# Kernel tuning notes

Hardware: AMD Instinct MI355X
Metric: run time of the kernel (lower is better)

The kernel has to match this reference:

```python
import jax, jax.numpy as jnp
import numpy as np

IN_FEATURES = 4096
OUT_FEATURES = 14336
GROUP_SIZE = 128
EPS = 1e-6


def setup_inputs() -> dict:
    key = jax.random.key(0)
    k1, k2, k3, k4 = jax.random.split(key, 4)
    num_groups = IN_FEATURES // GROUP_SIZE
    x = jax.random.normal(k1, (8, IN_FEATURES), dtype=jnp.float32)
    weights_uint8 = jax.random.randint(k2, (OUT_FEATURES, IN_FEATURES), 0, 256, dtype=jnp.int32)
    # per-(out_row, group) [scale, min_val]; scale small so dequant weights are O(1)
    scales_min_vals = jax.random.normal(k3, (OUT_FEATURES * num_groups, 2), dtype=jnp.float32) * 0.01
    norm_weights = jnp.ones((IN_FEATURES,), dtype=jnp.float32)
    bias = jax.random.normal(k4, (OUT_FEATURES,), dtype=jnp.float32)
    return {
        "x": x,
        "weights_uint8": weights_uint8,
        "scales_min_vals": scales_min_vals,
        "norm_weights": norm_weights,
        "bias": bias,
    }


def _dequantize(weights_uint8, scales_min_vals):
    out_f, in_f = weights_uint8.shape
    ng = in_f // GROUP_SIZE
    smv = scales_min_vals.reshape(out_f, ng, 2)  # [O, G, 2]
    wq = weights_uint8.reshape(out_f, ng, GROUP_SIZE).astype(jnp.float32)
    # RTN dequant: w = q * scale + min_val, per group
    w = wq * smv[..., 0:1] + smv[..., 1:2]
    return w.reshape(out_f, in_f)


def _rmsnorm(x, norm_weights):
    var = jnp.mean(x * x, axis=-1, keepdims=True)
    return x * jax.lax.rsqrt(var + EPS) * norm_weights


def reference(x, weights_uint8, scales_min_vals, norm_weights, bias):
    xn = _rmsnorm(x, norm_weights)               # [B, I]
    w = _dequantize(weights_uint8, scales_min_vals)  # [O, I]
    return jnp.einsum('bi,oi->bo', xn, w) + bias  # [B, O]
```

## Files before the change

kernel.cpp:

```cpp
#include <hip/hip_runtime.h>

#define IN_F 4096
#define OUT_F 14336
#define NG 32
#define NB 8

__global__ __launch_bounds__(256) void rmsnorm_k(const float* __restrict__ x,
                                                 const float* __restrict__ nw,
                                                 float* __restrict__ xn) {
  const int b = blockIdx.x;
  const int t = threadIdx.x;
  const float* xr = x + b * IN_F;
  float4 v[4];
  float ss = 0.f;
#pragma unroll
  for (int i = 0; i < 4; ++i) {
    v[i] = reinterpret_cast<const float4*>(xr)[i * 256 + t];
    ss += v[i].x * v[i].x + v[i].y * v[i].y + v[i].z * v[i].z + v[i].w * v[i].w;
  }
#pragma unroll
  for (int m = 1; m < 64; m <<= 1) ss += __shfl_xor(ss, m, 64);
  __shared__ float red[4];
  if ((t & 63) == 0) red[t >> 6] = ss;
  __syncthreads();
  ss = red[0] + red[1] + red[2] + red[3];
  const float r = rsqrtf(ss * (1.0f / IN_F) + 1e-6f);
#pragma unroll
  for (int i = 0; i < 4; ++i) {
    float4 w = reinterpret_cast<const float4*>(nw)[i * 256 + t];
    float4 o;
    o.x = v[i].x * r * w.x;
    o.y = v[i].y * r * w.y;
    o.z = v[i].z * r * w.z;
    o.w = v[i].w * r * w.w;
    reinterpret_cast<float4*>(xn + b * IN_F)[i * 256 + t] = o;
  }
}

__global__ __launch_bounds__(256) void gemv_k(const int* __restrict__ W,
                                              const float2* __restrict__ smv,
                                              const float* __restrict__ xn,
                                              const float* __restrict__ bias,
                                              float* __restrict__ out) {
  const int t = threadIdx.x;
  const int lane = t & 63;
  const int wave = t >> 6;
  const int row0 = (blockIdx.x * 4 + wave) * 4;

  float acc[4][NB];
#pragma unroll
  for (int rr = 0; rr < 4; ++rr)
#pragma unroll
    for (int b = 0; b < NB; ++b) acc[rr][b] = 0.f;

  const int lcol = lane * 4;
  for (int k = 0; k < 16; ++k) {
    const int col = k * 256 + lcol;
    float4 xv[NB];
#pragma unroll
    for (int b = 0; b < NB; ++b)
      xv[b] = *reinterpret_cast<const float4*>(xn + b * IN_F + col);
    const int g = col >> 7;
#pragma unroll
    for (int rr = 0; rr < 4; ++rr) {
      const int o = row0 + rr;
      const int4 q = *reinterpret_cast<const int4*>(W + o * IN_F + col);
      const float2 sm = smv[o * NG + g];
      const float w0 = (float)q.x * sm.x + sm.y;
      const float w1 = (float)q.y * sm.x + sm.y;
      const float w2 = (float)q.z * sm.x + sm.y;
      const float w3 = (float)q.w * sm.x + sm.y;
#pragma unroll
      for (int b = 0; b < NB; ++b) {
        acc[rr][b] = fmaf(w0, xv[b].x, acc[rr][b]);
        acc[rr][b] = fmaf(w1, xv[b].y, acc[rr][b]);
        acc[rr][b] = fmaf(w2, xv[b].z, acc[rr][b]);
        acc[rr][b] = fmaf(w3, xv[b].w, acc[rr][b]);
      }
    }
  }

#pragma unroll
  for (int rr = 0; rr < 4; ++rr)
#pragma unroll
    for (int b = 0; b < NB; ++b) {
      float v = acc[rr][b];
#pragma unroll
      for (int m = 1; m < 64; m <<= 1) v += __shfl_xor(v, m, 64);
      acc[rr][b] = v;
    }

  if (lane < 32) {
    const int rr = lane >> 3;
    const int b = lane & 7;
    const int o = row0 + rr;
    out[b * OUT_F + o] = acc[rr][b] + bias[o];
  }
}

extern "C" void kernel_launch(void* const* d_in, const int* in_sizes, int n_in,
                              void* d_out, int out_size, void* d_ws, size_t ws_size,
                              hipStream_t stream) {
  const float* x = (const float*)d_in[0];
  const int* W = (const int*)d_in[1];
  const float2* smv = (const float2*)d_in[2];
  const float* nw = (const float*)d_in[3];
  const float* bias = (const float*)d_in[4];
  float* out = (float*)d_out;
  float* xn = (float*)d_ws;

  rmsnorm_k<<<NB, 256, 0, stream>>>(x, nw, xn);
  gemv_k<<<OUT_F / 16, 256, 0, stream>>>(W, smv, xn, bias, out);
}
```

Baseline: 348.3 us.

## Raise rows per wave, use nontemporal weight loads, reduce via shared memory

```diff
diff --git a/kernel.cpp b/kernel.cpp
--- a/kernel.cpp
+++ b/kernel.cpp
@@ -4,52 +4,50 @@
 #define OUT_F 14336
 #define NG 32
 #define NB 8
+#define RPW 7
+#define RPB 28
+#define NBLK 512
 
-__global__ __launch_bounds__(256) void rmsnorm_k(const float* __restrict__ x,
-                                                 const float* __restrict__ nw,
-                                                 float* __restrict__ xn) {
+typedef int v4i __attribute__((ext_vector_type(4)));
+
+__global__ __launch_bounds__(1024) void rmsnorm_k(const float* __restrict__ x,
+                                                  const float* __restrict__ nw,
+                                                  float* __restrict__ xn) {
   const int b = blockIdx.x;
   const int t = threadIdx.x;
-  const float* xr = x + b * IN_F;
-  float4 v[4];
-  float ss = 0.f;
-#pragma unroll
-  for (int i = 0; i < 4; ++i) {
-    v[i] = reinterpret_cast<const float4*>(xr)[i * 256 + t];
-    ss += v[i].x * v[i].x + v[i].y * v[i].y + v[i].z * v[i].z + v[i].w * v[i].w;
-  }
+  float4 v = reinterpret_cast<const float4*>(x + b * IN_F)[t];
+  float ss = v.x * v.x + v.y * v.y + v.z * v.z + v.w * v.w;
 #pragma unroll
   for (int m = 1; m < 64; m <<= 1) ss += __shfl_xor(ss, m, 64);
-  __shared__ float red[4];
+  __shared__ float red[16];
   if ((t & 63) == 0) red[t >> 6] = ss;
   __syncthreads();
-  ss = red[0] + red[1] + red[2] + red[3];
-  const float r = rsqrtf(ss * (1.0f / IN_F) + 1e-6f);
+  float tot = 0.f;
 #pragma unroll
-  for (int i = 0; i < 4; ++i) {
-    float4 w = reinterpret_cast<const float4*>(nw)[i * 256 + t];
-    float4 o;
-    o.x = v[i].x * r * w.x;
-    o.y = v[i].y * r * w.y;
-    o.z = v[i].z * r * w.z;
-    o.w = v[i].w * r * w.w;
-    reinterpret_cast<float4*>(xn + b * IN_F)[i * 256 + t] = o;
-  }
+  for (int i = 0; i < 16; ++i) tot += red[i];
+  const float r = rsqrtf(tot * (1.0f / IN_F) + 1e-6f);
+  float4 w = reinterpret_cast<const float4*>(nw)[t];
+  float4 o;
+  o.x = v.x * r * w.x;
+  o.y = v.y * r * w.y;
+  o.z = v.z * r * w.z;
+  o.w = v.w * r * w.w;
+  reinterpret_cast<float4*>(xn + b * IN_F)[t] = o;
 }
 
-__global__ __launch_bounds__(256) void gemv_k(const int* __restrict__ W,
-                                              const float2* __restrict__ smv,
-                                              const float* __restrict__ xn,
-                                              const float* __restrict__ bias,
-                                              float* __restrict__ out) {
+__global__ __launch_bounds__(256, 2) void gemv_k(const int* __restrict__ W,
+                                                 const float2* __restrict__ smv,
+                                                 const float* __restrict__ xn,
+                                                 const float* __restrict__ bias,
+                                                 float* __restrict__ out) {
   const int t = threadIdx.x;
   const int lane = t & 63;
   const int wave = t >> 6;
-  const int row0 = (blockIdx.x * 4 + wave) * 4;
+  const int row0 = blockIdx.x * RPB + wave * RPW;
 
-  float acc[4][NB];
+  float acc[RPW][NB];
 #pragma unroll
-  for (int rr = 0; rr < 4; ++rr)
+  for (int rr = 0; rr < RPW; ++rr)
 #pragma unroll
     for (int b = 0; b < NB; ++b) acc[rr][b] = 0.f;
 
@@ -62,14 +60,15 @@
       xv[b] = *reinterpret_cast<const float4*>(xn + b * IN_F + col);
     const int g = col >> 7;
 #pragma unroll
-    for (int rr = 0; rr < 4; ++rr) {
+    for (int rr = 0; rr < RPW; ++rr) {
       const int o = row0 + rr;
-      const int4 q = *reinterpret_cast<const int4*>(W + o * IN_F + col);
+      const v4i q = __builtin_nontemporal_load(
+          reinterpret_cast<const v4i*>(W + o * IN_F + col));
       const float2 sm = smv[o * NG + g];
-      const float w0 = (float)q.x * sm.x + sm.y;
-      const float w1 = (float)q.y * sm.x + sm.y;
-      const float w2 = (float)q.z * sm.x + sm.y;
-      const float w3 = (float)q.w * sm.x + sm.y;
+      const float w0 = fmaf((float)q.x, sm.x, sm.y);
+      const float w1 = fmaf((float)q.y, sm.x, sm.y);
+      const float w2 = fmaf((float)q.z, sm.x, sm.y);
+      const float w3 = fmaf((float)q.w, sm.x, sm.y);
 #pragma unroll
       for (int b = 0; b < NB; ++b) {
         acc[rr][b] = fmaf(w0, xv[b].x, acc[rr][b]);
@@ -80,21 +79,27 @@
     }
   }
 
+  __shared__ float p[64][225];
 #pragma unroll
-  for (int rr = 0; rr < 4; ++rr)
+  for (int rr = 0; rr < RPW; ++rr)
 #pragma unroll
-    for (int b = 0; b < NB; ++b) {
-      float v = acc[rr][b];
+    for (int b = 0; b < NB; ++b)
+      p[lane][wave * (RPW * NB) + rr * NB + b] = acc[rr][b];
+  __syncthreads();
+
+  if (t < RPB * NB) {
+    float s0 = 0.f, s1 = 0.f, s2 = 0.f, s3 = 0.f;
 #pragma unroll
-      for (int m = 1; m < 64; m <<= 1) v += __shfl_xor(v, m, 64);
-      acc[rr][b] = v;
+    for (int l = 0; l < 64; l += 4) {
+      s0 += p[l + 0][t];
+      s1 += p[l + 1][t];
+      s2 += p[l + 2][t];
+      s3 += p[l + 3][t];
     }
-
-  if (lane < 32) {
-    const int rr = lane >> 3;
-    const int b = lane & 7;
-    const int o = row0 + rr;
-    out[b * OUT_F + o] = acc[rr][b] + bias[o];
+    const int r = t >> 3;
+    const int b = t & 7;
+    const int o = blockIdx.x * RPB + r;
+    out[b * OUT_F + o] = (s0 + s1) + (s2 + s3) + bias[o];
   }
 }
 
@@ -109,6 +114,6 @@
   float* out = (float*)d_out;
   float* xn = (float*)d_ws;
 
-  rmsnorm_k<<<NB, 256, 0, stream>>>(x, nw, xn);
-  gemv_k<<<OUT_F / 16, 256, 0, stream>>>(W, smv, xn, bias, out);
+  rmsnorm_k<<<NB, 1024, 0, stream>>>(x, nw, xn);
+  gemv_k<<<NBLK, 256, 0, stream>>>(W, smv, xn, bias, out);
 }
```

Result: faster. 314.8 us (-9.6%).
